# Kernel optimization log

Measured on AMD Instinct MI355X. Metric: run time of the kernel, lower is better.

## Reference

```python
import jax, jax.numpy as jnp
import numpy as np

N_HEADS = 8


def _update_state(demand, dyn, idx, cap0):
    # subtract demand of chosen node; reset to full capacity when returning to depot (node 0)
    cur = jnp.take_along_axis(demand, idx[:, None], axis=1)  # (B,1)
    dyn = dyn - cur
    dyn = jnp.where((idx == 0)[:, None], cap0, dyn)
    return jax.lax.stop_gradient(dyn)  # mirrors .detach() in the torch repo


def _update_mask(demand, dyn, idx, mask1):
    B, N = demand.shape
    go_depot = (idx == 0)
    mask1 = mask1.at[jnp.arange(B), idx].set(1.0)          # mark visited
    depot_mask = go_depot.astype(mask1.dtype)              # cannot stay at depot
    done = mask1[:, 1:].sum(axis=1) >= (N - 1)             # all customers served
    depot_mask = jnp.where(done, jnp.zeros_like(depot_mask), depot_mask)
    mask1 = mask1.at[:, 0].set(depot_mask)
    mask = jnp.minimum(mask1 + (demand > dyn).astype(mask1.dtype), 1.0)
    mask = mask.at[:, 0].set(depot_mask)                   # depot never capacity-masked
    return mask, mask1


def _pointer_logits(state_t, context, mask, T, wq, wk, wv, wo, wkp):
    # multi-head glimpse + single-head tanh-clipped pointer (Kool/Lei-style)
    B, N, D = context.shape
    H = wq.shape[1]
    hd = H // N_HEADS
    q = (state_t @ wq).reshape(B, N_HEADS, hd)
    k = (context @ wk).reshape(B, N, N_HEADS, hd)
    v = (context @ wv).reshape(B, N, N_HEADS, hd)
    u = jnp.einsum('bhd,bnhd->bhn', q, k) * (hd ** -0.5)   # (B,H,N)
    u = jnp.where(mask[:, None, :] > 0, -jnp.inf, u)
    a = jax.nn.softmax(u, axis=-1)
    glimpse = jnp.einsum('bhn,bnhd->bhd', a, v).reshape(B, H) @ wo  # (B,H)
    kp = context @ wkp                                     # (B,N,H)
    comp = jnp.einsum('bd,bnd->bn', glimpse, kp) * (H ** -0.5)
    logits = 10.0 * jnp.tanh(comp) / T
    return jnp.where(mask > 0, -jnp.inf, logits)           # (B,N)


def _decode(encoder_inputs, pool, capacity, demand, fc_w, fc1_w, wq, wk, wv, wo, wkp, T, n_steps, num_samples, greedy):
    B, N, D = encoder_inputs.shape
    cap0 = capacity[0, 0]
    base_key = jax.random.key(1234)
    actions_all, logps_all = [], []
    for s in range(num_samples):
        mask1 = jnp.zeros((B, N), encoder_inputs.dtype)
        dyn = jnp.broadcast_to(capacity, (B, 1)).astype(encoder_inputs.dtype)
        idx0 = jnp.zeros((B,), jnp.int32)
        mask, mask1 = _update_mask(demand, dyn, idx0, mask1)   # i == 0 pre-mask
        inp = encoder_inputs[:, 0, :]

        def step(carry, key):
            inp, dyn, mask, mask1, pool = carry
            dec = jnp.concatenate([inp, dyn], axis=-1) @ fc_w  # fc
            pool = pool @ fc1_w  # NB: fc1 re-applied to pool EVERY step (faithful quirk of source)
            dec = dec + pool
            logits = _pointer_logits(dec, encoder_inputs, mask, T, wq, wk, wv, wo, wkp)
            if greedy:
                idx = jnp.argmax(logits, axis=-1).astype(jnp.int32)
            else:
                idx = jax.random.categorical(key, logits).astype(jnp.int32)
            log_p = jnp.take_along_axis(jax.nn.log_softmax(logits, axis=-1), idx[:, None], axis=1)[:, 0]
            dyn = _update_state(demand, dyn, idx, cap0)
            mask, mask1 = _update_mask(demand, dyn, idx, mask1)
            # faithful to source: compares against full seq_len, so is_done is always 0
            is_done = (mask1[:, 1:].sum(axis=1) >= N).astype(log_p.dtype)
            log_p = log_p * (1.0 - is_done)
            inp = jnp.take_along_axis(encoder_inputs, idx[:, None, None], axis=1)[:, 0, :]
            return (inp, dyn, mask, mask1, pool), (idx, log_p)

        keys = jax.random.split(jax.random.fold_in(base_key, s), n_steps)
        (inp, dyn, mask, mask1, pool), (acts, lps) = jax.lax.scan(
            step, (inp, dyn, mask, mask1, pool), keys)
        actions_all.append(acts.T)          # (B, n_steps)
        logps_all.append(lps.sum(axis=0))   # (B,)
    return jnp.stack(actions_all), jnp.stack(logps_all)


def setup_inputs() -> dict:
    key = jax.random.key(0)
    ks = jax.random.split(key, 10)
    B, N, D = 256, 51, 128
    H = D
    s = 0.08  # ~ xavier std for 128x128
    enc = jax.random.normal(ks[0], (B, N, D), jnp.float32)
    pool = jax.random.normal(ks[1], (B, H), jnp.float32)
    capacity = jnp.ones((1, 1), jnp.float32)
    demand = jax.random.uniform(ks[2], (B, N), jnp.float32) * 0.3
    demand = demand.at[:, 0].set(0.0)  # depot has no demand
    return dict(
        encoder_inputs=enc, pool=pool, capacity=capacity, demand=demand,
        fc_w=jax.random.normal(ks[3], (H + 1, H), jnp.float32) * s,
        fc1_w=jax.random.normal(ks[4], (H, H), jnp.float32) * s,
        wq=jax.random.normal(ks[5], (H, H), jnp.float32) * s,
        wk=jax.random.normal(ks[6], (D, H), jnp.float32) * s,
        wv=jax.random.normal(ks[7], (D, H), jnp.float32) * s,
        wo=jax.random.normal(ks[8], (H, H), jnp.float32) * s,
        wkp=jax.random.normal(ks[9], (D, H), jnp.float32) * s,
        T=jnp.asarray(1.0, jnp.float32), n_steps=60, num_samples=1, greedy=0)


def reference(encoder_inputs, pool, capacity, demand, fc_w, fc1_w, wq, wk, wv, wo, wkp, T, n_steps, num_samples, greedy):
    return _decode(encoder_inputs, pool, capacity, demand, fc_w, fc1_w, wq, wk, wv, wo, wkp,
                   T, n_steps, num_samples, greedy)
```

## Files before the change

kernel.cpp:

```cpp
#include <hip/hip_runtime.h>

#define NN 51
#define DD 128
#define RS 132
#define NT 64
#define NINFF (-__builtin_inff())

__device__ __forceinline__ float dot4(const float4 a, const float4 b) {
  return a.x * b.x + a.y * b.y + a.z * b.z + a.w * b.w;
}

template<int CTRL>
__device__ __forceinline__ float dppf(float x, float idf) {
  return __int_as_float(__builtin_amdgcn_update_dpp(
      __float_as_int(idf), __float_as_int(x), CTRL, 0xf, 0xf, false));
}
__device__ __forceinline__ float readlanef(float x, int lane) {
  return __int_as_float(__builtin_amdgcn_readlane(__float_as_int(x), lane));
}
__device__ __forceinline__ float bcast63(float x) { return readlanef(x, 63); }
__device__ __forceinline__ float wave_max_b(float x) {
  x = fmaxf(x, dppf<0x111>(x, NINFF));
  x = fmaxf(x, dppf<0x112>(x, NINFF));
  x = fmaxf(x, dppf<0x114>(x, NINFF));
  x = fmaxf(x, dppf<0x118>(x, NINFF));
  x = fmaxf(x, dppf<0x142>(x, NINFF));
  x = fmaxf(x, dppf<0x143>(x, NINFF));
  return bcast63(x);
}
__device__ __forceinline__ float wave_sum_b(float x) {
  x += dppf<0x111>(x, 0.f);
  x += dppf<0x112>(x, 0.f);
  x += dppf<0x114>(x, 0.f);
  x += dppf<0x118>(x, 0.f);
  x += dppf<0x142>(x, 0.f);
  x += dppf<0x143>(x, 0.f);
  return bcast63(x);
}
__device__ __forceinline__ float row16_sum(float x) {
  x += dppf<0x111>(x, 0.f);
  x += dppf<0x112>(x, 0.f);
  x += dppf<0x114>(x, 0.f);
  x += dppf<0x118>(x, 0.f);
  return x;
}
__device__ __forceinline__ float quad_sum(float x) {
  x += dppf<0xB1>(x, 0.f);
  x += dppf<0x4E>(x, 0.f);
  return x;
}

__device__ __forceinline__ void tf2x32(unsigned k0, unsigned k1, unsigned &x0, unsigned &x1) {
  const unsigned ks2 = k0 ^ k1 ^ 0x1BD11BDAu;
  const unsigned ka[5] = {k1, ks2, k0, k1, ks2};
  const unsigned kb[5] = {ks2 + 1u, k0 + 2u, k1 + 3u, ks2 + 4u, k0 + 5u};
  x0 += k0; x1 += k1;
#pragma unroll
  for (int g = 0; g < 5; ++g) {
    const int r0 = (g & 1) ? 17 : 13;
    const int r1 = (g & 1) ? 29 : 15;
    const int r2 = (g & 1) ? 16 : 26;
    const int r3 = (g & 1) ? 24 : 6;
    x0 += x1; x1 = (x1 << r0) | (x1 >> (32 - r0)); x1 ^= x0;
    x0 += x1; x1 = (x1 << r1) | (x1 >> (32 - r1)); x1 ^= x0;
    x0 += x1; x1 = (x1 << r2) | (x1 >> (32 - r2)); x1 ^= x0;
    x0 += x1; x1 = (x1 << r3) | (x1 >> (32 - r3)); x1 ^= x0;
    x0 += ka[g]; x1 += kb[g];
  }
}

__device__ __forceinline__ float gumbel_from(unsigned k0, unsigned k1, unsigned ctr) {
  unsigned x0 = 0u, x1 = ctr;
  tf2x32(k0, k1, x0, x1);
  const unsigned bits = x0 ^ x1;
  const float fl = __uint_as_float((bits >> 9) | 0x3f800000u) - 1.0f;
  const float TINY = 1.17549435e-38f;
  const float uu = fmaxf(TINY, fl + TINY);
  return -logf(-logf(uu));
}

__global__ __launch_bounds__(512, 1) void decode_kernel(
    const float* __restrict__ enc, const float* __restrict__ pool_in,
    const float* __restrict__ cap_p, const float* __restrict__ demand,
    const float* __restrict__ fc_w, const float* __restrict__ fc1,
    const float* __restrict__ wq, const float* __restrict__ wk,
    const float* __restrict__ wv, const float* __restrict__ wo,
    const float* __restrict__ wkp, const float* __restrict__ T_p,
    const int* __restrict__ ns_p, const int* __restrict__ greedy_p,
    float* __restrict__ out) {
  __shared__ __align__(16) float Ksh[NN * RS];
  __shared__ __align__(16) float Vsh[52 * RS];
  __shared__ __align__(16) float KP2sh[NN * RS];
  __shared__ __align__(16) float EQsh[NN * RS];
  __shared__ __align__(16) float qpoolL[NT * DD];
  __shared__ __align__(16) float pcb2[2][8 * 64];
  __shared__ __align__(16) float poolB[2][DD];
  __shared__ __align__(16) float wrowL[DD];
  __shared__ __align__(16) float gumT[NT * NN];
  __shared__ float demL[NN];
  __shared__ float actsL[NT];
  __shared__ unsigned keysL[2 * NT];

  const int b = blockIdx.x, tid = threadIdx.x;
  const int Bn = gridDim.x;
  const int w = tid >> 6, l = tid & 63;
  int ns = *ns_p; if (ns > NT) ns = NT;
  const int greedy = *greedy_p;
  const float Tval = *T_p;
  const float cap0 = *cap_p;
  float* partF = &pcb2[0][0];

  {
    const float4* src = (const float4*)(enc + (size_t)b * NN * DD);
    float4* dst = (float4*)qpoolL;
    for (int e = tid; e < NN * DD / 4; e += 512) dst[e] = src[e];
  }
  if (tid < 128) poolB[0][tid] = pool_in[b * DD + tid];
  if (tid < RS)  Vsh[51 * RS + tid] = 0.f;
  if (tid < NN)  demL[tid] = demand[b * NN + tid];
  if (tid < ns) {
    unsigned a0 = 0u, a1 = 0u;
    tf2x32(0u, 1234u, a0, a1);
    unsigned x0 = 0u, x1 = (unsigned)tid;
    tf2x32(a0, a1, x0, x1);
    keysL[2 * tid] = x0; keysL[2 * tid + 1] = x1;
  }
  __syncthreads();

  float dem_l = (l < NN) ? demL[l] : 0.f;

  if (!greedy) {
    for (int job = tid; job < ns * NN; job += 512) {
      const int t = job / NN, n = job - t * NN;
      gumT[job] = gumbel_from(keysL[2 * t], keysL[2 * t + 1], (unsigned)(b * NN + n));
    }
  }
  {
    const int c = tid & 127, qd = tid >> 7;
    const float* fr = fc_w + 128 * DD;
    float s = 0.f;
    for (int j = qd * 32; j < qd * 32 + 32; ++j) s += fr[j] * wq[j * DD + c];
    partF[tid] = s;
  }
  __syncthreads();
  if (tid < 128)
    wrowL[tid] = partF[tid] + partF[tid + 128] + partF[tid + 256] + partF[tid + 384];

  const int g4 = tid >> 7, cc = tid & 127;
  const int n0 = g4 * 13, cnt13 = (g4 == 3) ? 12 : 13;

  {
    float aK[13], aV[13], aT1[13], aT2[13];
#pragma unroll
    for (int r = 0; r < 13; ++r) { aK[r] = 0.f; aV[r] = 0.f; aT1[r] = 0.f; aT2[r] = 0.f; }
    for (int i = 0; i < DD; i += 4) {
      const float k0 = wk[(i + 0) * DD + cc], k1 = wk[(i + 1) * DD + cc];
      const float k2 = wk[(i + 2) * DD + cc], k3 = wk[(i + 3) * DD + cc];
      const float v0 = wv[(i + 0) * DD + cc], v1 = wv[(i + 1) * DD + cc];
      const float v2 = wv[(i + 2) * DD + cc], v3 = wv[(i + 3) * DD + cc];
      const float f0 = fc_w[(i + 0) * DD + cc], f1 = fc_w[(i + 1) * DD + cc];
      const float f2 = fc_w[(i + 2) * DD + cc], f3 = fc_w[(i + 3) * DD + cc];
      const float p0 = wkp[(i + 0) * DD + cc], p1 = wkp[(i + 1) * DD + cc];
      const float p2 = wkp[(i + 2) * DD + cc], p3 = wkp[(i + 3) * DD + cc];
#pragma unroll
      for (int r = 0; r < 13; ++r) {
        if (r < cnt13) {
          const float4 e4 = *(const float4*)&qpoolL[(n0 + r) * DD + i];
          aK[r]  += e4.x * k0 + e4.y * k1 + e4.z * k2 + e4.w * k3;
          aV[r]  += e4.x * v0 + e4.y * v1 + e4.z * v2 + e4.w * v3;
          aT1[r] += e4.x * f0 + e4.y * f1 + e4.z * f2 + e4.w * f3;
          aT2[r] += e4.x * p0 + e4.y * p1 + e4.z * p2 + e4.w * p3;
        }
      }
    }
#pragma unroll
    for (int r = 0; r < 13; ++r) {
      if (r < cnt13) {
        Ksh[(n0 + r) * RS + cc]   = aK[r];
        Vsh[(n0 + r) * RS + cc]   = aV[r];
        EQsh[(n0 + r) * RS + cc]  = aT1[r];
        KP2sh[(n0 + r) * RS + cc] = aT2[r];
      }
    }
  }
  __syncthreads();

  {
    float aEQ[13], aKP[13];
#pragma unroll
    for (int r = 0; r < 13; ++r) { aEQ[r] = 0.f; aKP[r] = 0.f; }
    for (int i = 0; i < DD; i += 4) {
      const float q0 = wq[(i + 0) * DD + cc], q1 = wq[(i + 1) * DD + cc];
      const float q2 = wq[(i + 2) * DD + cc], q3 = wq[(i + 3) * DD + cc];
      const float4 w4 = *(const float4*)&wo[cc * DD + i];
#pragma unroll
      for (int r = 0; r < 13; ++r) {
        if (r < cnt13) {
          const float4 t1 = *(const float4*)&EQsh[(n0 + r) * RS + i];
          const float4 t2 = *(const float4*)&KP2sh[(n0 + r) * RS + i];
          aEQ[r] += t1.x * q0 + t1.y * q1 + t1.z * q2 + t1.w * q3;
          aKP[r] += dot4(t2, w4);
        }
      }
    }
    __syncthreads();
#pragma unroll
    for (int r = 0; r < 13; ++r) {
      if (r < cnt13) {
        EQsh[(n0 + r) * RS + cc]  = aEQ[r];
        KP2sh[(n0 + r) * RS + cc] = aKP[r];
      }
    }
  }
  __syncthreads();

  const int rowc = (l < NN) ? l : 0;
  const float4* kbase = (const float4*)&Ksh[rowc * RS + w * 16];
  const float4 Kr0 = kbase[0], Kr1 = kbase[1], Kr2 = kbase[2], Kr3 = kbase[3];
  const float4* pbase = (const float4*)&KP2sh[rowc * RS + w * 16];
  const float4 Pr0 = pbase[0], Pr1 = pbase[1], Pr2 = pbase[2], Pr3 = pbase[3];
  const int nn0 = l & 15, dq = l >> 4;
  const int vr3 = (nn0 + 48 <= 51) ? (nn0 + 48) : 51;
  const float4 Vr0 = *(const float4*)&Vsh[(nn0 +  0) * RS + w * 16 + dq * 4];
  const float4 Vr1 = *(const float4*)&Vsh[(nn0 + 16) * RS + w * 16 + dq * 4];
  const float4 Vr2 = *(const float4*)&Vsh[(nn0 + 32) * RS + w * 16 + dq * 4];
  const float4 Vr3 = *(const float4*)&Vsh[vr3 * RS + w * 16 + dq * 4];
  const float4* wbase = (const float4*)&wrowL[w * 16];
  const float4 Wr0 = wbase[0], Wr1 = wbase[1], Wr2 = wbase[2], Wr3 = wbase[3];

  {
    const int colC = tid >> 2, qrt = tid & 3;
    float wfr[32];
#pragma unroll
    for (int i = 0; i < 32; ++i) wfr[i] = fc1[(qrt * 32 + i) * DD + colC];
    int cur = 0;
    for (int t = 0; t < ns; ++t) {
      float s = 0.f;
#pragma unroll
      for (int i = 0; i < 32; ++i) s += poolB[cur][qrt * 32 + i] * wfr[i];
      s = quad_sum(s);
      if (qrt == 0) {
        qpoolL[t * DD + colC] = s;
        poolB[cur ^ 1][colC] = s;
      }
      cur ^= 1;
      __syncthreads();
    }
    const int qch = (ns + 3) >> 2;
    const int r0 = g4 * qch;
    const int rcnt = (ns - r0 < qch) ? (ns - r0) : qch;
    float acc[16];
#pragma unroll
    for (int r = 0; r < 16; ++r) acc[r] = 0.f;
    for (int i = 0; i < DD; i += 4) {
      const float q0 = wq[(i + 0) * DD + cc], q1 = wq[(i + 1) * DD + cc];
      const float q2 = wq[(i + 2) * DD + cc], q3 = wq[(i + 3) * DD + cc];
#pragma unroll
      for (int r = 0; r < 16; ++r) {
        if (r < rcnt) {
          const float4 p4 = *(const float4*)&qpoolL[(r0 + r) * DD + i];
          acc[r] += p4.x * q0 + p4.y * q1 + p4.z * q2 + p4.w * q3;
        }
      }
    }
    __syncthreads();
#pragma unroll
    for (int r = 0; r < 16; ++r)
      if (r < rcnt) qpoolL[(r0 + r) * DD + cc] = acc[r];
  }
  __syncthreads();

  int m1 = (l == 0) ? 1 : 0;
  float dynr = cap0, depotr = 1.f, lpacc0 = 0.f, lpacc1 = 0.f;
  float4 qv0, qv1, qv2, qv3;
  {
    const float4* eq = (const float4*)&EQsh[0 * RS + w * 16];
    const float4* qp = (const float4*)&qpoolL[0 * DD + w * 16];
    qv0.x = eq[0].x + cap0 * Wr0.x + qp[0].x; qv0.y = eq[0].y + cap0 * Wr0.y + qp[0].y;
    qv0.z = eq[0].z + cap0 * Wr0.z + qp[0].z; qv0.w = eq[0].w + cap0 * Wr0.w + qp[0].w;
    qv1.x = eq[1].x + cap0 * Wr1.x + qp[1].x; qv1.y = eq[1].y + cap0 * Wr1.y + qp[1].y;
    qv1.z = eq[1].z + cap0 * Wr1.z + qp[1].z; qv1.w = eq[1].w + cap0 * Wr1.w + qp[1].w;
    qv2.x = eq[2].x + cap0 * Wr2.x + qp[2].x; qv2.y = eq[2].y + cap0 * Wr2.y + qp[2].y;
    qv2.z = eq[2].z + cap0 * Wr2.z + qp[2].z; qv2.w = eq[2].w + cap0 * Wr2.w + qp[2].w;
    qv3.x = eq[3].x + cap0 * Wr3.x + qp[3].x; qv3.y = eq[3].y + cap0 * Wr3.y + qp[3].y;
    qv3.z = eq[3].z + cap0 * Wr3.z + qp[3].z; qv3.w = eq[3].w + cap0 * Wr3.w + qp[3].w;
  }

  for (int t = 0; t < ns; ++t) {
    {
      const bool maskedl =
          (l == 0) ? (depotr > 0.f)
          : (l < NN ? ((m1 != 0) || (dem_l > dynr)) : true);
      float u1 = NINFF;
      if (l < NN && !maskedl)
        u1 = 0.25f * ((dot4(Kr0, qv0) + dot4(Kr1, qv1)) +
                      (dot4(Kr2, qv2) + dot4(Kr3, qv3)));
      const float mx = wave_max_b(u1);
      const float e = (u1 > NINFF) ? expf(u1 - mx) : 0.f;
      const float a0 = __shfl(e, nn0);
      const float a1 = __shfl(e, nn0 + 16);
      const float a2 = __shfl(e, nn0 + 32);
      const float a3 = __shfl(e, nn0 + 48);
      const float S = wave_sum_b(e);
      float ax = a0 * Vr0.x + a1 * Vr1.x + a2 * Vr2.x + a3 * Vr3.x;
      float ay = a0 * Vr0.y + a1 * Vr1.y + a2 * Vr2.y + a3 * Vr3.y;
      float az = a0 * Vr0.z + a1 * Vr1.z + a2 * Vr2.z + a3 * Vr3.z;
      float aw = a0 * Vr0.w + a1 * Vr1.w + a2 * Vr2.w + a3 * Vr3.w;
      ax = row16_sum(ax) / S; ay = row16_sum(ay) / S;
      az = row16_sum(az) / S; aw = row16_sum(aw) / S;
      const float g0  = readlanef(ax, 15), g1  = readlanef(ay, 15);
      const float g2  = readlanef(az, 15), g3  = readlanef(aw, 15);
      const float g4g = readlanef(ax, 31), g5  = readlanef(ay, 31);
      const float g6  = readlanef(az, 31), g7  = readlanef(aw, 31);
      const float g8  = readlanef(ax, 47), g9  = readlanef(ay, 47);
      const float g10 = readlanef(az, 47), g11 = readlanef(aw, 47);
      const float g12 = readlanef(ax, 63), g13 = readlanef(ay, 63);
      const float g14 = readlanef(az, 63), g15 = readlanef(aw, 63);
      const float part =
          ((Pr0.x * g0  + Pr0.y * g1  + Pr0.z * g2  + Pr0.w * g3) +
           (Pr1.x * g4g + Pr1.y * g5  + Pr1.z * g6  + Pr1.w * g7)) +
          ((Pr2.x * g8  + Pr2.y * g9  + Pr2.z * g10 + Pr2.w * g11) +
           (Pr3.x * g12 + Pr3.y * g13 + Pr3.z * g14 + Pr3.w * g15));
      pcb2[t & 1][w * 64 + l] = part;
    }
    __syncthreads();
    {
      const int qidx = (t + 1 < ns) ? (t + 1) : 0;
      const float4* qp = (const float4*)&qpoolL[qidx * DD + w * 16];
      const float4 qp0 = qp[0], qp1 = qp[1], qp2 = qp[2], qp3 = qp[3];
      const float pg = (!greedy && l < NN) ? gumT[t * NN + l] : 0.f;
      const float* pcb = pcb2[t & 1];
      float lgv = NINFF;
      {
        const float p0 = pcb[0 * 64 + l], p1 = pcb[1 * 64 + l];
        const float p2 = pcb[2 * 64 + l], p3 = pcb[3 * 64 + l];
        const float p4 = pcb[4 * 64 + l], p5 = pcb[5 * 64 + l];
        const float p6 = pcb[6 * 64 + l], p7 = pcb[7 * 64 + l];
        const float comp = (((p0 + p1) + (p2 + p3)) + ((p4 + p5) + (p6 + p7))) *
                           0.08838834764831845f;
        const float lg = (10.f * tanhf(comp)) / Tval;
        const bool maskedn =
            (l == 0) ? (depotr > 0.f) : ((m1 != 0) || (dem_l > dynr));
        if (l < NN) lgv = maskedn ? NINFF : lg;
      }
      const float pv = (l < NN) ? (lgv + pg) : NINFF;
      const float vmax = wave_max_b(pv);
      const unsigned long long Meq = __ballot(pv == vmax);
      const int best = __ffsll(Meq) - 1;
      if (l == best) m1 = 1;
      const unsigned long long M = __ballot(m1 != 0);
      const int cntv = (int)__popcll(M & ~1ull);
      const float dem_b = readlanef(dem_l, best);
      dynr = (best == 0) ? cap0 : (dynr - dem_b);
      depotr = (best == 0) ? 1.f : 0.f;
      if (cntv >= NN - 1) depotr = 0.f;
      if (w == 1) {
        lpacc0 += readlanef(lgv, best);
        const float mm = wave_max_b(lgv);
        const float ee = wave_sum_b((lgv > NINFF) ? expf(lgv - mm) : 0.f);
        lpacc1 += mm + logf(ee);
      }
      if (w == 0 && l == 0) actsL[t] = (float)best;
      const float4* eq = (const float4*)&EQsh[best * RS + w * 16];
      qv0.x = eq[0].x + dynr * Wr0.x + qp0.x; qv0.y = eq[0].y + dynr * Wr0.y + qp0.y;
      qv0.z = eq[0].z + dynr * Wr0.z + qp0.z; qv0.w = eq[0].w + dynr * Wr0.w + qp0.w;
      qv1.x = eq[1].x + dynr * Wr1.x + qp1.x; qv1.y = eq[1].y + dynr * Wr1.y + qp1.y;
      qv1.z = eq[1].z + dynr * Wr1.z + qp1.z; qv1.w = eq[1].w + dynr * Wr1.w + qp1.w;
      qv2.x = eq[2].x + dynr * Wr2.x + qp2.x; qv2.y = eq[2].y + dynr * Wr2.y + qp2.y;
      qv2.z = eq[2].z + dynr * Wr2.z + qp2.z; qv2.w = eq[2].w + dynr * Wr2.w + qp2.w;
      qv3.x = eq[3].x + dynr * Wr3.x + qp3.x; qv3.y = eq[3].y + dynr * Wr3.y + qp3.y;
      qv3.z = eq[3].z + dynr * Wr3.z + qp3.z; qv3.w = eq[3].w + dynr * Wr3.w + qp3.w;
    }
  }
  __syncthreads();
  if (w == 0 && l < ns) out[b * ns + l] = actsL[l];
  if (w == 1 && l == 0) out[Bn * ns + b] = lpacc0 - lpacc1;
}

extern "C" void kernel_launch(void* const* d_in, const int* in_sizes, int n_in,
                              void* d_out, int out_size, void* d_ws, size_t ws_size,
                              hipStream_t stream) {
  const float* enc    = (const float*)d_in[0];
  const float* pool   = (const float*)d_in[1];
  const float* cap    = (const float*)d_in[2];
  const float* dem    = (const float*)d_in[3];
  const float* fc_w   = (const float*)d_in[4];
  const float* fc1_w  = (const float*)d_in[5];
  const float* wq     = (const float*)d_in[6];
  const float* wk     = (const float*)d_in[7];
  const float* wv     = (const float*)d_in[8];
  const float* wo     = (const float*)d_in[9];
  const float* wkp    = (const float*)d_in[10];
  const float* Tp     = (const float*)d_in[11];
  const int*   nsp    = (const int*)d_in[12];
  const int*   greedy = (const int*)d_in[14];
  float* out = (float*)d_out;

  const int B = in_sizes[1] / DD;

  hipLaunchKernelGGL(decode_kernel, dim3(B), dim3(512), 0, stream,
                     enc, pool, cap, dem, fc_w, fc1_w, wq, wk, wv, wo, wkp,
                     Tp, nsp, greedy, out);
}
```

Before: 197.9 us.

## Double block to 1024 threads and offload log-prob reduction to extra wave

Launches 1024 threads per block instead of 512, so the precompute projections split node rows across 8 groups (7 rows each) and the fc1/pool recurrence uses 8-way partial sums with a new 8-lane DPP reduction. In the decode loop, waves 0-7 do the attention work, while a ninth wave now takes over the log-softmax accumulation that wave 1 used to do, which takes that reduction off the critical path. It also swaps the per-component division for a multiply by a reciprocal. The aim is more parallelism in the setup matmuls and a shorter serial step. The cost is higher register pressure under a 1024-thread launch bound and more idle waves waiting at each barrier.

```diff
diff --git a/kernel.cpp b/kernel.cpp
--- a/kernel.cpp
+++ b/kernel.cpp
@@ -44,9 +44,10 @@
   x += dppf<0x118>(x, 0.f);
   return x;
 }
-__device__ __forceinline__ float quad_sum(float x) {
+__device__ __forceinline__ float grp8_sum(float x) {
   x += dppf<0xB1>(x, 0.f);
   x += dppf<0x4E>(x, 0.f);
+  x += dppf<0x141>(x, 0.f);
   return x;
 }
 
@@ -79,7 +80,7 @@
   return -logf(-logf(uu));
 }
 
-__global__ __launch_bounds__(512, 1) void decode_kernel(
+__global__ __launch_bounds__(1024, 1) void decode_kernel(
     const float* __restrict__ enc, const float* __restrict__ pool_in,
     const float* __restrict__ cap_p, const float* __restrict__ demand,
     const float* __restrict__ fc_w, const float* __restrict__ fc1,
@@ -108,12 +109,11 @@
   const int greedy = *greedy_p;
   const float Tval = *T_p;
   const float cap0 = *cap_p;
-  float* partF = &pcb2[0][0];
 
   {
     const float4* src = (const float4*)(enc + (size_t)b * NN * DD);
     float4* dst = (float4*)qpoolL;
-    for (int e = tid; e < NN * DD / 4; e += 512) dst[e] = src[e];
+    for (int e = tid; e < NN * DD / 4; e += 1024) dst[e] = src[e];
   }
   if (tid < 128) poolB[0][tid] = pool_in[b * DD + tid];
   if (tid < RS)  Vsh[51 * RS + tid] = 0.f;
@@ -130,29 +130,32 @@
   float dem_l = (l < NN) ? demL[l] : 0.f;
 
   if (!greedy) {
-    for (int job = tid; job < ns * NN; job += 512) {
+    for (int job = tid; job < ns * NN; job += 1024) {
       const int t = job / NN, n = job - t * NN;
       gumT[job] = gumbel_from(keysL[2 * t], keysL[2 * t + 1], (unsigned)(b * NN + n));
     }
   }
   {
-    const int c = tid & 127, qd = tid >> 7;
+    const int c = tid >> 3, qrt = tid & 7;
     const float* fr = fc_w + 128 * DD;
     float s = 0.f;
-    for (int j = qd * 32; j < qd * 32 + 32; ++j) s += fr[j] * wq[j * DD + c];
-    partF[tid] = s;
-  }
-  __syncthreads();
-  if (tid < 128)
-    wrowL[tid] = partF[tid] + partF[tid + 128] + partF[tid + 256] + partF[tid + 384];
-
-  const int g4 = tid >> 7, cc = tid & 127;
-  const int n0 = g4 * 13, cnt13 = (g4 == 3) ? 12 : 13;
+#pragma unroll
+    for (int i = 0; i < 16; ++i) {
+      const int j = qrt * 16 + i;
+      s += fr[j] * wq[j * DD + c];
+    }
+    s = grp8_sum(s);
+    if (qrt == 0) wrowL[c] = s;
+  }
+
+  const int g8 = tid >> 7, cc = tid & 127;
+  const int n0 = g8 * 7;
+  const int cnt7 = (n0 + 7 <= NN) ? 7 : (NN - n0);
 
   {
-    float aK[13], aV[13], aT1[13], aT2[13];
-#pragma unroll
-    for (int r = 0; r < 13; ++r) { aK[r] = 0.f; aV[r] = 0.f; aT1[r] = 0.f; aT2[r] = 0.f; }
+    float aK[7], aV[7], aT1[7], aT2[7];
+#pragma unroll
+    for (int r = 0; r < 7; ++r) { aK[r] = 0.f; aV[r] = 0.f; aT1[r] = 0.f; aT2[r] = 0.f; }
     for (int i = 0; i < DD; i += 4) {
       const float k0 = wk[(i + 0) * DD + cc], k1 = wk[(i + 1) * DD + cc];
       const float k2 = wk[(i + 2) * DD + cc], k3 = wk[(i + 3) * DD + cc];
@@ -163,8 +166,8 @@
       const float p0 = wkp[(i + 0) * DD + cc], p1 = wkp[(i + 1) * DD + cc];
       const float p2 = wkp[(i + 2) * DD + cc], p3 = wkp[(i + 3) * DD + cc];
 #pragma unroll
-      for (int r = 0; r < 13; ++r) {
-        if (r < cnt13) {
+      for (int r = 0; r < 7; ++r) {
+        if (r < cnt7) {
           const float4 e4 = *(const float4*)&qpoolL[(n0 + r) * DD + i];
           aK[r]  += e4.x * k0 + e4.y * k1 + e4.z * k2 + e4.w * k3;
           aV[r]  += e4.x * v0 + e4.y * v1 + e4.z * v2 + e4.w * v3;
@@ -174,8 +177,8 @@
       }
     }
 #pragma unroll
-    for (int r = 0; r < 13; ++r) {
-      if (r < cnt13) {
+    for (int r = 0; r < 7; ++r) {
+      if (r < cnt7) {
         Ksh[(n0 + r) * RS + cc]   = aK[r];
         Vsh[(n0 + r) * RS + cc]   = aV[r];
         EQsh[(n0 + r) * RS + cc]  = aT1[r];
@@ -186,16 +189,16 @@
   __syncthreads();
 
   {
-    float aEQ[13], aKP[13];
-#pragma unroll
-    for (int r = 0; r < 13; ++r) { aEQ[r] = 0.f; aKP[r] = 0.f; }
+    float aEQ[7], aKP[7];
+#pragma unroll
+    for (int r = 0; r < 7; ++r) { aEQ[r] = 0.f; aKP[r] = 0.f; }
     for (int i = 0; i < DD; i += 4) {
       const float q0 = wq[(i + 0) * DD + cc], q1 = wq[(i + 1) * DD + cc];
       const float q2 = wq[(i + 2) * DD + cc], q3 = wq[(i + 3) * DD + cc];
       const float4 w4 = *(const float4*)&wo[cc * DD + i];
 #pragma unroll
-      for (int r = 0; r < 13; ++r) {
-        if (r < cnt13) {
+      for (int r = 0; r < 7; ++r) {
+        if (r < cnt7) {
           const float4 t1 = *(const float4*)&EQsh[(n0 + r) * RS + i];
           const float4 t2 = *(const float4*)&KP2sh[(n0 + r) * RS + i];
           aEQ[r] += t1.x * q0 + t1.y * q1 + t1.z * q2 + t1.w * q3;
@@ -205,8 +208,8 @@
     }
     __syncthreads();
 #pragma unroll
-    for (int r = 0; r < 13; ++r) {
-      if (r < cnt13) {
+    for (int r = 0; r < 7; ++r) {
+      if (r < cnt7) {
         EQsh[(n0 + r) * RS + cc]  = aEQ[r];
         KP2sh[(n0 + r) * RS + cc] = aKP[r];
       }
@@ -214,31 +217,37 @@
   }
   __syncthreads();
 
-  const int rowc = (l < NN) ? l : 0;
-  const float4* kbase = (const float4*)&Ksh[rowc * RS + w * 16];
-  const float4 Kr0 = kbase[0], Kr1 = kbase[1], Kr2 = kbase[2], Kr3 = kbase[3];
-  const float4* pbase = (const float4*)&KP2sh[rowc * RS + w * 16];
-  const float4 Pr0 = pbase[0], Pr1 = pbase[1], Pr2 = pbase[2], Pr3 = pbase[3];
+  float4 Kr0{0,0,0,0}, Kr1{0,0,0,0}, Kr2{0,0,0,0}, Kr3{0,0,0,0};
+  float4 Pr0{0,0,0,0}, Pr1{0,0,0,0}, Pr2{0,0,0,0}, Pr3{0,0,0,0};
+  float4 Vr0{0,0,0,0}, Vr1{0,0,0,0}, Vr2{0,0,0,0}, Vr3{0,0,0,0};
+  float4 Wr0{0,0,0,0}, Wr1{0,0,0,0}, Wr2{0,0,0,0}, Wr3{0,0,0,0};
   const int nn0 = l & 15, dq = l >> 4;
-  const int vr3 = (nn0 + 48 <= 51) ? (nn0 + 48) : 51;
-  const float4 Vr0 = *(const float4*)&Vsh[(nn0 +  0) * RS + w * 16 + dq * 4];
-  const float4 Vr1 = *(const float4*)&Vsh[(nn0 + 16) * RS + w * 16 + dq * 4];
-  const float4 Vr2 = *(const float4*)&Vsh[(nn0 + 32) * RS + w * 16 + dq * 4];
-  const float4 Vr3 = *(const float4*)&Vsh[vr3 * RS + w * 16 + dq * 4];
-  const float4* wbase = (const float4*)&wrowL[w * 16];
-  const float4 Wr0 = wbase[0], Wr1 = wbase[1], Wr2 = wbase[2], Wr3 = wbase[3];
+  if (w < 8) {
+    const int rowc = (l < NN) ? l : 0;
+    const float4* kbase = (const float4*)&Ksh[rowc * RS + w * 16];
+    Kr0 = kbase[0]; Kr1 = kbase[1]; Kr2 = kbase[2]; Kr3 = kbase[3];
+    const float4* pbase = (const float4*)&KP2sh[rowc * RS + w * 16];
+    Pr0 = pbase[0]; Pr1 = pbase[1]; Pr2 = pbase[2]; Pr3 = pbase[3];
+    const int vr3 = (nn0 + 48 <= 51) ? (nn0 + 48) : 51;
+    Vr0 = *(const float4*)&Vsh[(nn0 +  0) * RS + w * 16 + dq * 4];
+    Vr1 = *(const float4*)&Vsh[(nn0 + 16) * RS + w * 16 + dq * 4];
+    Vr2 = *(const float4*)&Vsh[(nn0 + 32) * RS + w * 16 + dq * 4];
+    Vr3 = *(const float4*)&Vsh[vr3 * RS + w * 16 + dq * 4];
+    const float4* wbase = (const float4*)&wrowL[w * 16];
+    Wr0 = wbase[0]; Wr1 = wbase[1]; Wr2 = wbase[2]; Wr3 = wbase[3];
+  }
 
   {
-    const int colC = tid >> 2, qrt = tid & 3;
-    float wfr[32];
-#pragma unroll
-    for (int i = 0; i < 32; ++i) wfr[i] = fc1[(qrt * 32 + i) * DD + colC];
+    const int colC = tid >> 3, qrt = tid & 7;
+    float wfr[16];
+#pragma unroll
+    for (int i = 0; i < 16; ++i) wfr[i] = fc1[(qrt * 16 + i) * DD + colC];
     int cur = 0;
     for (int t = 0; t < ns; ++t) {
       float s = 0.f;
 #pragma unroll
-      for (int i = 0; i < 32; ++i) s += poolB[cur][qrt * 32 + i] * wfr[i];
-      s = quad_sum(s);
+      for (int i = 0; i < 16; ++i) s += poolB[cur][qrt * 16 + i] * wfr[i];
+      s = grp8_sum(s);
       if (qrt == 0) {
         qpoolL[t * DD + colC] = s;
         poolB[cur ^ 1][colC] = s;
@@ -246,34 +255,34 @@
       cur ^= 1;
       __syncthreads();
     }
-    const int qch = (ns + 3) >> 2;
-    const int r0 = g4 * qch;
-    const int rcnt = (ns - r0 < qch) ? (ns - r0) : qch;
-    float acc[16];
-#pragma unroll
-    for (int r = 0; r < 16; ++r) acc[r] = 0.f;
+    const int qch = (ns + 7) >> 3;
+    const int r0q = g8 * qch;
+    int rcnt = ns - r0q; if (rcnt > qch) rcnt = qch; if (rcnt < 0) rcnt = 0;
+    float acc[8];
+#pragma unroll
+    for (int r = 0; r < 8; ++r) acc[r] = 0.f;
     for (int i = 0; i < DD; i += 4) {
       const float q0 = wq[(i + 0) * DD + cc], q1 = wq[(i + 1) * DD + cc];
       const float q2 = wq[(i + 2) * DD + cc], q3 = wq[(i + 3) * DD + cc];
 #pragma unroll
-      for (int r = 0; r < 16; ++r) {
+      for (int r = 0; r < 8; ++r) {
         if (r < rcnt) {
-          const float4 p4 = *(const float4*)&qpoolL[(r0 + r) * DD + i];
+          const float4 p4 = *(const float4*)&qpoolL[(r0q + r) * DD + i];
           acc[r] += p4.x * q0 + p4.y * q1 + p4.z * q2 + p4.w * q3;
         }
       }
     }
     __syncthreads();
 #pragma unroll
-    for (int r = 0; r < 16; ++r)
-      if (r < rcnt) qpoolL[(r0 + r) * DD + cc] = acc[r];
+    for (int r = 0; r < 8; ++r)
+      if (r < rcnt) qpoolL[(r0q + r) * DD + cc] = acc[r];
   }
   __syncthreads();
 
   int m1 = (l == 0) ? 1 : 0;
   float dynr = cap0, depotr = 1.f, lpacc0 = 0.f, lpacc1 = 0.f;
   float4 qv0, qv1, qv2, qv3;
-  {
+  if (w < 8) {
     const float4* eq = (const float4*)&EQsh[0 * RS + w * 16];
     const float4* qp = (const float4*)&qpoolL[0 * DD + w * 16];
     qv0.x = eq[0].x + cap0 * Wr0.x + qp[0].x; qv0.y = eq[0].y + cap0 * Wr0.y + qp[0].y;
@@ -287,7 +296,7 @@
   }
 
   for (int t = 0; t < ns; ++t) {
-    {
+    if (w < 8) {
       const bool maskedl =
           (l == 0) ? (depotr > 0.f)
           : (l < NN ? ((m1 != 0) || (dem_l > dynr)) : true);
@@ -302,32 +311,30 @@
       const float a2 = __shfl(e, nn0 + 32);
       const float a3 = __shfl(e, nn0 + 48);
       const float S = wave_sum_b(e);
+      const float rS = 1.f / S;
       float ax = a0 * Vr0.x + a1 * Vr1.x + a2 * Vr2.x + a3 * Vr3.x;
       float ay = a0 * Vr0.y + a1 * Vr1.y + a2 * Vr2.y + a3 * Vr3.y;
       float az = a0 * Vr0.z + a1 * Vr1.z + a2 * Vr2.z + a3 * Vr3.z;
       float aw = a0 * Vr0.w + a1 * Vr1.w + a2 * Vr2.w + a3 * Vr3.w;
-      ax = row16_sum(ax) / S; ay = row16_sum(ay) / S;
-      az = row16_sum(az) / S; aw = row16_sum(aw) / S;
+      ax = row16_sum(ax) * rS; ay = row16_sum(ay) * rS;
+      az = row16_sum(az) * rS; aw = row16_sum(aw) * rS;
       const float g0  = readlanef(ax, 15), g1  = readlanef(ay, 15);
       const float g2  = readlanef(az, 15), g3  = readlanef(aw, 15);
       const float g4g = readlanef(ax, 31), g5  = readlanef(ay, 31);
       const float g6  = readlanef(az, 31), g7  = readlanef(aw, 31);
-      const float g8  = readlanef(ax, 47), g9  = readlanef(ay, 47);
+      const float g8r = readlanef(ax, 47), g9  = readlanef(ay, 47);
       const float g10 = readlanef(az, 47), g11 = readlanef(aw, 47);
       const float g12 = readlanef(ax, 63), g13 = readlanef(ay, 63);
       const float g14 = readlanef(az, 63), g15 = readlanef(aw, 63);
       const float part =
           ((Pr0.x * g0  + Pr0.y * g1  + Pr0.z * g2  + Pr0.w * g3) +
            (Pr1.x * g4g + Pr1.y * g5  + Pr1.z * g6  + Pr1.w * g7)) +
-          ((Pr2.x * g8  + Pr2.y * g9  + Pr2.z * g10 + Pr2.w * g11) +
+          ((Pr2.x * g8r + Pr2.y * g9  + Pr2.z * g10 + Pr2.w * g11) +
            (Pr3.x * g12 + Pr3.y * g13 + Pr3.z * g14 + Pr3.w * g15));
       pcb2[t & 1][w * 64 + l] = part;
     }
     __syncthreads();
-    {
-      const int qidx = (t + 1 < ns) ? (t + 1) : 0;
-      const float4* qp = (const float4*)&qpoolL[qidx * DD + w * 16];
-      const float4 qp0 = qp[0], qp1 = qp[1], qp2 = qp[2], qp3 = qp[3];
+    if (w <= 8) {
       const float pg = (!greedy && l < NN) ? gumT[t * NN + l] : 0.f;
       const float* pcb = pcb2[t & 1];
       float lgv = NINFF;
@@ -354,27 +361,31 @@
       dynr = (best == 0) ? cap0 : (dynr - dem_b);
       depotr = (best == 0) ? 1.f : 0.f;
       if (cntv >= NN - 1) depotr = 0.f;
-      if (w == 1) {
+      if (w == 8) {
         lpacc0 += readlanef(lgv, best);
         const float mm = wave_max_b(lgv);
         const float ee = wave_sum_b((lgv > NINFF) ? expf(lgv - mm) : 0.f);
         lpacc1 += mm + logf(ee);
-      }
-      if (w == 0 && l == 0) actsL[t] = (float)best;
-      const float4* eq = (const float4*)&EQsh[best * RS + w * 16];
-      qv0.x = eq[0].x + dynr * Wr0.x + qp0.x; qv0.y = eq[0].y + dynr * Wr0.y + qp0.y;
-      qv0.z = eq[0].z + dynr * Wr0.z + qp0.z; qv0.w = eq[0].w + dynr * Wr0.w + qp0.w;
-      qv1.x = eq[1].x + dynr * Wr1.x + qp1.x; qv1.y = eq[1].y + dynr * Wr1.y + qp1.y;
-      qv1.z = eq[1].z + dynr * Wr1.z + qp1.z; qv1.w = eq[1].w + dynr * Wr1.w + qp1.w;
-      qv2.x = eq[2].x + dynr * Wr2.x + qp2.x; qv2.y = eq[2].y + dynr * Wr2.y + qp2.y;
-      qv2.z = eq[2].z + dynr * Wr2.z + qp2.z; qv2.w = eq[2].w + dynr * Wr2.w + qp2.w;
-      qv3.x = eq[3].x + dynr * Wr3.x + qp3.x; qv3.y = eq[3].y + dynr * Wr3.y + qp3.y;
-      qv3.z = eq[3].z + dynr * Wr3.z + qp3.z; qv3.w = eq[3].w + dynr * Wr3.w + qp3.w;
+      } else {
+        if (w == 0 && l == 0) actsL[t] = (float)best;
+        const int qidx = (t + 1 < ns) ? (t + 1) : 0;
+        const float4* qp = (const float4*)&qpoolL[qidx * DD + w * 16];
+        const float4 qp0 = qp[0], qp1 = qp[1], qp2 = qp[2], qp3 = qp[3];
+        const float4* eq = (const float4*)&EQsh[best * RS + w * 16];
+        qv0.x = eq[0].x + dynr * Wr0.x + qp0.x; qv0.y = eq[0].y + dynr * Wr0.y + qp0.y;
+        qv0.z = eq[0].z + dynr * Wr0.z + qp0.z; qv0.w = eq[0].w + dynr * Wr0.w + qp0.w;
+        qv1.x = eq[1].x + dynr * Wr1.x + qp1.x; qv1.y = eq[1].y + dynr * Wr1.y + qp1.y;
+        qv1.z = eq[1].z + dynr * Wr1.z + qp1.z; qv1.w = eq[1].w + dynr * Wr1.w + qp1.w;
+        qv2.x = eq[2].x + dynr * Wr2.x + qp2.x; qv2.y = eq[2].y + dynr * Wr2.y + qp2.y;
+        qv2.z = eq[2].z + dynr * Wr2.z + qp2.z; qv2.w = eq[2].w + dynr * Wr2.w + qp2.w;
+        qv3.x = eq[3].x + dynr * Wr3.x + qp3.x; qv3.y = eq[3].y + dynr * Wr3.y + qp3.y;
+        qv3.z = eq[3].z + dynr * Wr3.z + qp3.z; qv3.w = eq[3].w + dynr * Wr3.w + qp3.w;
+      }
     }
   }
   __syncthreads();
   if (w == 0 && l < ns) out[b * ns + l] = actsL[l];
-  if (w == 1 && l == 0) out[Bn * ns + b] = lpacc0 - lpacc1;
+  if (w == 8 && l == 0) out[Bn * ns + b] = lpacc0 - lpacc1;
 }
 
 extern "C" void kernel_launch(void* const* d_in, const int* in_sizes, int n_in,
@@ -398,7 +409,7 @@
 
   const int B = in_sizes[1] / DD;
 
-  hipLaunchKernelGGL(decode_kernel, dim3(B), dim3(512), 0, stream,
+  hipLaunchKernelGGL(decode_kernel, dim3(B), dim3(1024), 0, stream,
                      enc, pool, cap, dem, fc_w, fc1_w, wq, wk, wv, wo, wkp,
                      Tp, nsp, greedy, out);
 }
```

After: 214.0 us. 8.2% more time.

## Defer per-step log-sum-exp to post-loop parallel pass; gather EQ via readlane

Applied to the files above, without the earlier changes.

Removes the per-step log-softmax normalizer (max, exp, sum, log) from wave 1 in the serial decode loop. Each step's logits are stored into the now-unused qpoolL buffer, and all 8 waves compute the log-sum-exp terms in parallel after the loop. The next query row is rebuilt by reading register-cached EQ values with readlane from the chosen lane instead of an LDS load indexed by best, and the softmax divides become one reciprocal plus multiplies. The cost is 16 extra registers per thread and a slightly different rounding order.

```diff
diff --git a/kernel.cpp b/kernel.cpp
--- a/kernel.cpp
+++ b/kernel.cpp
@@ -99,6 +99,7 @@
   __shared__ __align__(16) float gumT[NT * NN];
   __shared__ float demL[NN];
   __shared__ float actsL[NT];
+  __shared__ float lseP[8];
   __shared__ unsigned keysL[2 * NT];
 
   const int b = blockIdx.x, tid = threadIdx.x;
@@ -219,6 +220,9 @@
   const float4 Kr0 = kbase[0], Kr1 = kbase[1], Kr2 = kbase[2], Kr3 = kbase[3];
   const float4* pbase = (const float4*)&KP2sh[rowc * RS + w * 16];
   const float4 Pr0 = pbase[0], Pr1 = pbase[1], Pr2 = pbase[2], Pr3 = pbase[3];
+  float EQr[16];
+#pragma unroll
+  for (int j = 0; j < 16; ++j) EQr[j] = EQsh[rowc * RS + w * 16 + j];
   const int nn0 = l & 15, dq = l >> 4;
   const int vr3 = (nn0 + 48 <= 51) ? (nn0 + 48) : 51;
   const float4 Vr0 = *(const float4*)&Vsh[(nn0 +  0) * RS + w * 16 + dq * 4];
@@ -271,7 +275,7 @@
   __syncthreads();
 
   int m1 = (l == 0) ? 1 : 0;
-  float dynr = cap0, depotr = 1.f, lpacc0 = 0.f, lpacc1 = 0.f;
+  float dynr = cap0, depotr = 1.f, lpacc0 = 0.f;
   float4 qv0, qv1, qv2, qv3;
   {
     const float4* eq = (const float4*)&EQsh[0 * RS + w * 16];
@@ -302,12 +306,13 @@
       const float a2 = __shfl(e, nn0 + 32);
       const float a3 = __shfl(e, nn0 + 48);
       const float S = wave_sum_b(e);
+      const float rS = 1.f / S;
       float ax = a0 * Vr0.x + a1 * Vr1.x + a2 * Vr2.x + a3 * Vr3.x;
       float ay = a0 * Vr0.y + a1 * Vr1.y + a2 * Vr2.y + a3 * Vr3.y;
       float az = a0 * Vr0.z + a1 * Vr1.z + a2 * Vr2.z + a3 * Vr3.z;
       float aw = a0 * Vr0.w + a1 * Vr1.w + a2 * Vr2.w + a3 * Vr3.w;
-      ax = row16_sum(ax) / S; ay = row16_sum(ay) / S;
-      az = row16_sum(az) / S; aw = row16_sum(aw) / S;
+      ax = row16_sum(ax) * rS; ay = row16_sum(ay) * rS;
+      az = row16_sum(az) * rS; aw = row16_sum(aw) * rS;
       const float g0  = readlanef(ax, 15), g1  = readlanef(ay, 15);
       const float g2  = readlanef(az, 15), g3  = readlanef(aw, 15);
       const float g4g = readlanef(ax, 31), g5  = readlanef(ay, 31);
@@ -354,27 +359,48 @@
       dynr = (best == 0) ? cap0 : (dynr - dem_b);
       depotr = (best == 0) ? 1.f : 0.f;
       if (cntv >= NN - 1) depotr = 0.f;
-      if (w == 1) {
+      if (w == 0) {
+        if (l < NN) qpoolL[t * DD + l] = lgv;
         lpacc0 += readlanef(lgv, best);
-        const float mm = wave_max_b(lgv);
-        const float ee = wave_sum_b((lgv > NINFF) ? expf(lgv - mm) : 0.f);
-        lpacc1 += mm + logf(ee);
-      }
-      if (w == 0 && l == 0) actsL[t] = (float)best;
-      const float4* eq = (const float4*)&EQsh[best * RS + w * 16];
-      qv0.x = eq[0].x + dynr * Wr0.x + qp0.x; qv0.y = eq[0].y + dynr * Wr0.y + qp0.y;
-      qv0.z = eq[0].z + dynr * Wr0.z + qp0.z; qv0.w = eq[0].w + dynr * Wr0.w + qp0.w;
-      qv1.x = eq[1].x + dynr * Wr1.x + qp1.x; qv1.y = eq[1].y + dynr * Wr1.y + qp1.y;
-      qv1.z = eq[1].z + dynr * Wr1.z + qp1.z; qv1.w = eq[1].w + dynr * Wr1.w + qp1.w;
-      qv2.x = eq[2].x + dynr * Wr2.x + qp2.x; qv2.y = eq[2].y + dynr * Wr2.y + qp2.y;
-      qv2.z = eq[2].z + dynr * Wr2.z + qp2.z; qv2.w = eq[2].w + dynr * Wr2.w + qp2.w;
-      qv3.x = eq[3].x + dynr * Wr3.x + qp3.x; qv3.y = eq[3].y + dynr * Wr3.y + qp3.y;
-      qv3.z = eq[3].z + dynr * Wr3.z + qp3.z; qv3.w = eq[3].w + dynr * Wr3.w + qp3.w;
-    }
+        if (l == 0) actsL[t] = (float)best;
+      }
+      qv0.x = readlanef(EQr[ 0], best) + dynr * Wr0.x + qp0.x;
+      qv0.y = readlanef(EQr[ 1], best) + dynr * Wr0.y + qp0.y;
+      qv0.z = readlanef(EQr[ 2], best) + dynr * Wr0.z + qp0.z;
+      qv0.w = readlanef(EQr[ 3], best) + dynr * Wr0.w + qp0.w;
+      qv1.x = readlanef(EQr[ 4], best) + dynr * Wr1.x + qp1.x;
+      qv1.y = readlanef(EQr[ 5], best) + dynr * Wr1.y + qp1.y;
+      qv1.z = readlanef(EQr[ 6], best) + dynr * Wr1.z + qp1.z;
+      qv1.w = readlanef(EQr[ 7], best) + dynr * Wr1.w + qp1.w;
+      qv2.x = readlanef(EQr[ 8], best) + dynr * Wr2.x + qp2.x;
+      qv2.y = readlanef(EQr[ 9], best) + dynr * Wr2.y + qp2.y;
+      qv2.z = readlanef(EQr[10], best) + dynr * Wr2.z + qp2.z;
+      qv2.w = readlanef(EQr[11], best) + dynr * Wr2.w + qp2.w;
+      qv3.x = readlanef(EQr[12], best) + dynr * Wr3.x + qp3.x;
+      qv3.y = readlanef(EQr[13], best) + dynr * Wr3.y + qp3.y;
+      qv3.z = readlanef(EQr[14], best) + dynr * Wr3.z + qp3.z;
+      qv3.w = readlanef(EQr[15], best) + dynr * Wr3.w + qp3.w;
+    }
+  }
+  __syncthreads();
+
+  {
+    float lsum = 0.f;
+    for (int t = w; t < ns; t += 8) {
+      const float lv = (l < NN) ? qpoolL[t * DD + l] : NINFF;
+      const float mm = wave_max_b(lv);
+      const float ee = wave_sum_b((lv > NINFF) ? expf(lv - mm) : 0.f);
+      lsum += mm + logf(ee);
+    }
+    if (l == 0) lseP[w] = lsum;
   }
   __syncthreads();
   if (w == 0 && l < ns) out[b * ns + l] = actsL[l];
-  if (w == 1 && l == 0) out[Bn * ns + b] = lpacc0 - lpacc1;
+  if (w == 0 && l == 0) {
+    const float tot = ((lseP[0] + lseP[1]) + (lseP[2] + lseP[3])) +
+                      ((lseP[4] + lseP[5]) + (lseP[6] + lseP[7]));
+    out[Bn * ns + b] = lpacc0 - tot;
+  }
 }
 
 extern "C" void kernel_launch(void* const* d_in, const int* in_sizes, int n_in,
```

Measured after the change: 197.6 us. About the same (-0.1%).
